# Optimization experiments

Measured on AMD Instinct MI355X. Metric: run time of the kernel, lower is better.

Reference implementation:

```python
import jax, jax.numpy as jnp
import numpy as np

N, T, E, H, V = 32768, 20, 50, 50, 200
PAD = 0

def setup_inputs() -> dict:
    key = jax.random.key(0)
    ks = jax.random.split(key, 11)
    s = 1.0 / np.sqrt(H)  # torch LSTM init scale
    return {
        "char_indices": jax.random.randint(ks[0], (N, T), 0, V, dtype=jnp.int32),
        "word_lengths": jax.random.randint(ks[1], (N,), 0, T + 1, dtype=jnp.int32),
        "emb": jax.random.normal(ks[2], (V, E), jnp.float32) * 0.1,
        "W_ih_f": jax.random.normal(ks[3], (4 * H, E), jnp.float32) * s,
        "W_hh_f": jax.random.normal(ks[4], (4 * H, H), jnp.float32) * s,
        "b_ih_f": jax.random.normal(ks[5], (4 * H,), jnp.float32) * s,
        "b_hh_f": jax.random.normal(ks[6], (4 * H,), jnp.float32) * s,
        "W_ih_b": jax.random.normal(ks[7], (4 * H, E), jnp.float32) * s,
        "W_hh_b": jax.random.normal(ks[8], (4 * H, H), jnp.float32) * s,
        "b_ih_b": jax.random.normal(ks[9], (4 * H,), jnp.float32) * s,
        "b_hh_b": jax.random.normal(ks[10], (4 * H,), jnp.float32) * s,
    }

def _run_dir(x, lengths, W_ih, W_hh, b_ih, b_hh, reverse):
    # x: [N,T,E]; returns final hidden state [N,H] at the word's true boundary.
    n = x.shape[0]
    xg = jnp.einsum('nte,ge->ntg', x, W_ih) + b_ih + b_hh  # [N,T,4H]
    def step(carry, t):
        h, c = carry
        g = xg[:, t] + h @ W_hh.T  # [N,4H]
        i, f, gg, o = jnp.split(g, 4, axis=-1)
        c_new = jax.nn.sigmoid(f) * c + jax.nn.sigmoid(i) * jnp.tanh(gg)
        h_new = jax.nn.sigmoid(o) * jnp.tanh(c_new)
        valid = (t < lengths)[:, None]  # only update inside the word
        return (jnp.where(valid, h_new, h), jnp.where(valid, c_new, c)), None
    ts = jnp.arange(T - 1, -1, -1) if reverse else jnp.arange(T)
    z = jnp.zeros((n, W_hh.shape[1]), x.dtype)
    (h, _), _ = jax.lax.scan(step, (z, z), ts)
    return h

def reference(char_indices, word_lengths, emb, W_ih_f, W_hh_f, b_ih_f, b_hh_f,
              W_ih_b, W_hh_b, b_ih_b, b_hh_b):
    emb = emb.at[PAD].set(0.0)  # padding_idx row is zero
    x = emb[char_indices]  # [N,T,E]
    h_f = _run_dir(x, word_lengths, W_ih_f, W_hh_f, b_ih_f, b_hh_f, reverse=False)
    h_b = _run_dir(x, word_lengths, W_ih_b, W_hh_b, b_ih_b, b_hh_b, reverse=True)
    return jnp.concatenate([h_f, h_b], axis=-1)  # [N, 2H]
```

## Files before the change

### kernel.cpp

```cpp
#include <hip/hip_runtime.h>


#define TT    20
#define HH    50
#define VV    200
#define TILES 13
#define GSTR  212
#define GSH   (VV * GSTR)
#define WSH   (TILES * 16 * 64)
#define NW    32768
#define NB_G  332
#define NB_W  104
#define NB_H  128
#define NBLK  4096

#define N2LOG2E (-1.4426950408889634f)
#define P2LOG2E 2.8853900817779268f

typedef __attribute__((ext_vector_type(8))) short bf16x8;
typedef __attribute__((ext_vector_type(4))) short s16x4;
typedef __attribute__((ext_vector_type(4))) float f32x4;

__device__ __forceinline__ float frcp(float x) { return __builtin_amdgcn_rcpf(x); }
#if __has_builtin(__builtin_amdgcn_exp2f)
__device__ __forceinline__ float fexp2(float x) { return __builtin_amdgcn_exp2f(x); }
#else
__device__ __forceinline__ float fexp2(float x) { return exp2f(x); }
#endif

__device__ __forceinline__ short f2bf(float x) {
    unsigned b = __builtin_bit_cast(unsigned, x);
    unsigned r = (b + 0x7FFFu + ((b >> 16) & 1u)) >> 16;
    return (short)r;
}
__device__ __forceinline__ float bf2f(short s) {
    return __builtin_bit_cast(float, ((unsigned)(unsigned short)s) << 16);
}

__global__ void k_prep(const float* __restrict__ emb,
                       const float* __restrict__ Wih_f, const float* __restrict__ bih_f,
                       const float* __restrict__ bhh_f,
                       const float* __restrict__ Wih_b, const float* __restrict__ bih_b,
                       const float* __restrict__ bhh_b,
                       const float* __restrict__ Whh_f, const float* __restrict__ Whh_b,
                       const int* __restrict__ lens,
                       short* __restrict__ Gimg, short* __restrict__ Wimg,
                       int* __restrict__ cnt) {
    int blk = blockIdx.x;
    int tid = threadIdx.x;
    if (blk < NB_G) {
        int idx = blk * 256 + tid;
        if (idx >= 2 * GSH) return;
        int d = idx / GSH;
        int rem = idx % GSH;
        int v = rem / GSTR;
        int u = (rem % GSTR) >> 2;
        int g = idx & 3;
        if (u >= HH) { Gimg[idx] = 0; return; }
        int r = g * HH + u;
        const float* Wih = d ? Wih_b : Wih_f;
        const float* bih = d ? bih_b : bih_f;
        const float* bhh = d ? bhh_b : bhh_f;
        float s = bih[r] + bhh[r];
        if (v != 0) {
            #pragma unroll 10
            for (int e = 0; e < HH; ++e) s = fmaf(emb[v * HH + e], Wih[r * HH + e], s);
        }
        float sc = (g == 2) ? P2LOG2E : N2LOG2E;
        Gimg[idx] = f2bf(s * sc);
    } else if (blk < NB_G + NB_W) {
        int idx = (blk - NB_G) * 256 + tid;
        if (idx >= 2 * WSH) return;
        int d = idx / WSH;
        int e = idx % WSH;
        int t = e >> 10, m = (e >> 6) & 15, k = e & 63;
        int u = 4 * t + (m >> 2), g = m & 3;
        const float* Whh = d ? Whh_b : Whh_f;
        float sc = (g == 2) ? P2LOG2E : N2LOG2E;
        float val = (k < HH && u < HH) ? Whh[(g * HH + u) * HH + k] * sc : 0.0f;
        int ksw = (k & 7) | (((k >> 3) ^ (m & 7)) << 3);
        Wimg[d * WSH + (e & ~63) + ksw] = f2bf(val);
    } else {
        int hb = blk - NB_G - NB_W;
        __shared__ int hcnt[21];
        if (tid < 21) hcnt[tid] = 0;
        __syncthreads();
        atomicAdd(&hcnt[lens[hb * 256 + tid]], 1);
        __syncthreads();
        if (tid < 21) cnt[hb * 21 + tid] = hcnt[tid];
    }
}

__global__ void k_scat(const int* __restrict__ lens, const int* __restrict__ cnt,
                       int* __restrict__ perm) {
    __shared__ int lcnt[NB_H * 21];
    __shared__ int part[8][21];
    __shared__ int tot[21];
    __shared__ int cur[21];
    int b = blockIdx.x, t = threadIdx.x;
    for (int i = t; i < NB_H * 21; i += 256) lcnt[i] = cnt[i];
    __syncthreads();
    if (t < 168) {
        int L = t % 21, c = t / 21;
        int s = 0;
        for (int bb = c * 16; bb < c * 16 + 16; ++bb) s += lcnt[bb * 21 + L];
        part[c][L] = s;
    }
    __syncthreads();
    if (t < 21) {
        int a = 0;
        #pragma unroll
        for (int c = 0; c < 8; ++c) a += part[c][t];
        tot[t] = a;
    }
    __syncthreads();
    if (t < 21) {
        int a = 0;
        for (int L2 = 20; L2 > t; --L2) a += tot[L2];
        for (int bb = 0; bb < b; ++bb) a += lcnt[bb * 21 + t];
        cur[t] = a;
    }
    __syncthreads();
    int i = b * 256 + t;
    int pos = atomicAdd(&cur[lens[i]], 1);
    perm[pos] = i;
}

__launch_bounds__(512, 6)
__global__ void k_lstm(const int* __restrict__ chars, const int* __restrict__ lens,
                       const int* __restrict__ perm,
                       const short* __restrict__ Gimg, const short* __restrict__ Wimg,
                       float* __restrict__ out) {
    __shared__ __align__(16) short hs[2][1024];
    __shared__ unsigned char cs[16 * TT];

    int gb   = blockIdx.x;
    int d    = gb & 1;
    int grp  = gb >> 1;
    int tid  = threadIdx.x;
    int lane = tid & 63;
    int wv   = __builtin_amdgcn_readfirstlane(tid >> 6);
    int quad = lane >> 4;
    int n    = lane & 15;
    int x7   = n & 7;
    int slotbase = grp * 16;

    {
        int4 z = {0, 0, 0, 0};
        int4* hz = (int4*)&hs[0][0];
        if (tid < 256) hz[tid] = z;
    }
    for (int i = tid; i < 16 * TT; i += 512) {
        int w = perm[slotbase + i / TT];
        cs[i] = (unsigned char)chars[w * TT + i % TT];
    }

    int word = perm[slotbase + n];
    int L = lens[word];
    int mL = L;
    #pragma unroll
    for (int off = 8; off; off >>= 1) {
        int t2 = __shfl_xor(mL, off);
        mL = mL > t2 ? mL : t2;
    }
    mL = __builtin_amdgcn_readfirstlane(mL);

    int pa0 = quad ^ x7;
    int pa1 = (quad + 4) ^ x7;

    int tA = wv, tB = wv + 8;
    int nt = (wv < 5) ? 2 : 1;
    int uA = 4 * tA + quad;
    int uB = 4 * tB + quad;
    int hidxA = n * 64 + (((uA >> 3) ^ x7) << 3) + (uA & 7);
    int hidxB = n * 64 + (((uB >> 3) ^ x7) << 3) + (uB & 7);

    const short* Wd = Wimg + d * WSH;
    bf16x8 A0a = *(const bf16x8*)(Wd + (tA * 16 + n) * 64 + pa0 * 8);
    bf16x8 A1a = *(const bf16x8*)(Wd + (tA * 16 + n) * 64 + pa1 * 8);
    bf16x8 A0b, A1b;
    if (nt == 2) {
        A0b = *(const bf16x8*)(Wd + (tB * 16 + n) * 64 + pa0 * 8);
        A1b = *(const bf16x8*)(Wd + (tB * 16 + n) * 64 + pa1 * 8);
    }

    const short* Gg = Gimg + d * GSH;
    const unsigned char* cw = cs + n * TT;

    float cstA = 0.0f, hfA = 0.0f, cstB = 0.0f, hfB = 0.0f;

    __syncthreads();

    int vcur = cw[(d && L > 0) ? (L - 1) : 0];
    int cur = 0;

    #pragma unroll 1
    for (int s = 0; s < mL; ++s) {
        bool valid = s < L;

        const short* gvp = Gg + vcur * GSTR + quad * 4;
        s16x4 gvA = *(const s16x4*)(gvp + tA * 16);
        s16x4 gvB;
        if (nt == 2) gvB = *(const s16x4*)(gvp + tB * 16);

        const short* hb = hs[cur];
        bf16x8 B0 = *(const bf16x8*)(hb + n * 64 + pa0 * 8);
        bf16x8 B1 = *(const bf16x8*)(hb + n * 64 + pa1 * 8);

        int sn = s + 1;
        int pn = (sn < L) ? (d ? (L - 1 - sn) : sn) : 0;
        vcur = cw[pn];

        f32x4 aA;
        aA[0] = bf2f(gvA[0]); aA[1] = bf2f(gvA[1]);
        aA[2] = bf2f(gvA[2]); aA[3] = bf2f(gvA[3]);
        aA = __builtin_amdgcn_mfma_f32_16x16x32_bf16(A0a, B0, aA, 0, 0, 0);
        aA = __builtin_amdgcn_mfma_f32_16x16x32_bf16(A1a, B1, aA, 0, 0, 0);
        f32x4 aB;
        if (nt == 2) {
            aB[0] = bf2f(gvB[0]); aB[1] = bf2f(gvB[1]);
            aB[2] = bf2f(gvB[2]); aB[3] = bf2f(gvB[3]);
            aB = __builtin_amdgcn_mfma_f32_16x16x32_bf16(A0b, B0, aB, 0, 0, 0);
            aB = __builtin_amdgcn_mfma_f32_16x16x32_bf16(A1b, B1, aB, 0, 0, 0);
        }

        {
            float ig = frcp(1.0f + fexp2(aA[0]));
            float fg = frcp(1.0f + fexp2(aA[1]));
            float tg = 1.0f - 2.0f * frcp(1.0f + fexp2(aA[2]));
            float og = frcp(1.0f + fexp2(aA[3]));
            float cn = fg * cstA + ig * tg;
            float hn = og * (1.0f - 2.0f * frcp(1.0f + fexp2(cn * P2LOG2E)));
            bool upd = valid && (uA < HH);
            cstA = upd ? cn : cstA;
            hfA  = upd ? hn : hfA;
        }
        if (nt == 2) {
            float ig = frcp(1.0f + fexp2(aB[0]));
            float fg = frcp(1.0f + fexp2(aB[1]));
            float tg = 1.0f - 2.0f * frcp(1.0f + fexp2(aB[2]));
            float og = frcp(1.0f + fexp2(aB[3]));
            float cn = fg * cstB + ig * tg;
            float hn = og * (1.0f - 2.0f * frcp(1.0f + fexp2(cn * P2LOG2E)));
            bool upd = valid && (uB < HH);
            cstB = upd ? cn : cstB;
            hfB  = upd ? hn : hfB;
        }

        short* hnb = hs[cur ^ 1];
        if (uA < HH) hnb[hidxA] = f2bf(hfA);
        if (nt == 2 && uB < HH) hnb[hidxB] = f2bf(hfB);
        __syncthreads();
        cur ^= 1;
    }

    float* orow = out + (size_t)word * (2 * HH) + d * HH;
    if (uA < HH) orow[uA] = hfA;
    if (nt == 2 && uB < HH) orow[uB] = hfB;
}

extern "C" void kernel_launch(void* const* d_in, const int* in_sizes, int n_in,
                              void* d_out, int out_size, void* d_ws, size_t ws_size,
                              hipStream_t stream) {
    const int*   chars = (const int*)d_in[0];
    const int*   lens  = (const int*)d_in[1];
    const float* emb   = (const float*)d_in[2];
    const float* Wih_f = (const float*)d_in[3];
    const float* Whh_f = (const float*)d_in[4];
    const float* bih_f = (const float*)d_in[5];
    const float* bhh_f = (const float*)d_in[6];
    const float* Wih_b = (const float*)d_in[7];
    const float* Whh_b = (const float*)d_in[8];
    const float* bih_b = (const float*)d_in[9];
    const float* bhh_b = (const float*)d_in[10];
    float* out = (float*)d_out;

    short* Gimg = (short*)d_ws;
    short* Wimg = Gimg + 2 * GSH;
    int*   cnt  = (int*)(Wimg + 2 * WSH);
    int*   perm = cnt + NB_H * 21;

    k_prep<<<NB_G + NB_W + NB_H, 256, 0, stream>>>(emb, Wih_f, bih_f, bhh_f,
                                                   Wih_b, bih_b, bhh_b,
                                                   Whh_f, Whh_b, lens,
                                                   Gimg, Wimg, cnt);
    k_scat<<<NB_H, 256, 0, stream>>>(lens, cnt, perm);
    k_lstm<<<NBLK, 512, 0, stream>>>(chars, lens, perm, Gimg, Wimg, out);
}
```

Measured before the change: 146.3 us.

## Merge prep and scatter kernels via cooperative grid sync; resize LSTM blocks to 7 waves

The prep and scatter kernels become a single cooperative kernel that uses a grid-wide sync between histogram building and the permutation scatter, removing one launch. The LSTM kernel now runs 7 waves per block instead of 8, with the 13 hidden-unit tiles redistributed (tB = wv+7, six waves take two tiles) and launch bounds of 448 threads, 7 blocks. This aims to cut launch gaps and improve occupancy or balance, but the grid sync costs something and the cooperative launch needs all 564 blocks resident at once.

```diff
diff --git a/kernel.cpp b/kernel.cpp
--- a/kernel.cpp
+++ b/kernel.cpp
@@ -1,4 +1,5 @@
 #include <hip/hip_runtime.h>
+#include <hip/hip_cooperative_groups.h>
 
 
 #define TT    20
@@ -37,96 +38,103 @@
     return __builtin_bit_cast(float, ((unsigned)(unsigned short)s) << 16);
 }
 
-__global__ void k_prep(const float* __restrict__ emb,
-                       const float* __restrict__ Wih_f, const float* __restrict__ bih_f,
-                       const float* __restrict__ bhh_f,
-                       const float* __restrict__ Wih_b, const float* __restrict__ bih_b,
-                       const float* __restrict__ bhh_b,
-                       const float* __restrict__ Whh_f, const float* __restrict__ Whh_b,
-                       const int* __restrict__ lens,
-                       short* __restrict__ Gimg, short* __restrict__ Wimg,
-                       int* __restrict__ cnt) {
+__global__ void k_pre(const float* __restrict__ emb,
+                      const float* __restrict__ Wih_f, const float* __restrict__ bih_f,
+                      const float* __restrict__ bhh_f,
+                      const float* __restrict__ Wih_b, const float* __restrict__ bih_b,
+                      const float* __restrict__ bhh_b,
+                      const float* __restrict__ Whh_f, const float* __restrict__ Whh_b,
+                      const int* __restrict__ lens,
+                      short* __restrict__ Gimg, short* __restrict__ Wimg,
+                      int* __restrict__ cnt, int* __restrict__ perm) {
     int blk = blockIdx.x;
     int tid = threadIdx.x;
-    if (blk < NB_G) {
-        int idx = blk * 256 + tid;
-        if (idx >= 2 * GSH) return;
-        int d = idx / GSH;
-        int rem = idx % GSH;
-        int v = rem / GSTR;
-        int u = (rem % GSTR) >> 2;
-        int g = idx & 3;
-        if (u >= HH) { Gimg[idx] = 0; return; }
-        int r = g * HH + u;
-        const float* Wih = d ? Wih_b : Wih_f;
-        const float* bih = d ? bih_b : bih_f;
-        const float* bhh = d ? bhh_b : bhh_f;
-        float s = bih[r] + bhh[r];
-        if (v != 0) {
-            #pragma unroll 10
-            for (int e = 0; e < HH; ++e) s = fmaf(emb[v * HH + e], Wih[r * HH + e], s);
-        }
-        float sc = (g == 2) ? P2LOG2E : N2LOG2E;
-        Gimg[idx] = f2bf(s * sc);
-    } else if (blk < NB_G + NB_W) {
-        int idx = (blk - NB_G) * 256 + tid;
-        if (idx >= 2 * WSH) return;
-        int d = idx / WSH;
-        int e = idx % WSH;
-        int t = e >> 10, m = (e >> 6) & 15, k = e & 63;
-        int u = 4 * t + (m >> 2), g = m & 3;
-        const float* Whh = d ? Whh_b : Whh_f;
-        float sc = (g == 2) ? P2LOG2E : N2LOG2E;
-        float val = (k < HH && u < HH) ? Whh[(g * HH + u) * HH + k] * sc : 0.0f;
-        int ksw = (k & 7) | (((k >> 3) ^ (m & 7)) << 3);
-        Wimg[d * WSH + (e & ~63) + ksw] = f2bf(val);
-    } else {
-        int hb = blk - NB_G - NB_W;
-        __shared__ int hcnt[21];
-        if (tid < 21) hcnt[tid] = 0;
-        __syncthreads();
-        atomicAdd(&hcnt[lens[hb * 256 + tid]], 1);
-        __syncthreads();
-        if (tid < 21) cnt[hb * 21 + tid] = hcnt[tid];
-    }
-}
-
-__global__ void k_scat(const int* __restrict__ lens, const int* __restrict__ cnt,
-                       int* __restrict__ perm) {
     __shared__ int lcnt[NB_H * 21];
     __shared__ int part[8][21];
     __shared__ int tot[21];
     __shared__ int cur[21];
-    int b = blockIdx.x, t = threadIdx.x;
-    for (int i = t; i < NB_H * 21; i += 256) lcnt[i] = cnt[i];
-    __syncthreads();
-    if (t < 168) {
-        int L = t % 21, c = t / 21;
-        int s = 0;
-        for (int bb = c * 16; bb < c * 16 + 16; ++bb) s += lcnt[bb * 21 + L];
-        part[c][L] = s;
-    }
-    __syncthreads();
-    if (t < 21) {
-        int a = 0;
-        #pragma unroll
-        for (int c = 0; c < 8; ++c) a += part[c][t];
-        tot[t] = a;
-    }
-    __syncthreads();
-    if (t < 21) {
-        int a = 0;
-        for (int L2 = 20; L2 > t; --L2) a += tot[L2];
-        for (int bb = 0; bb < b; ++bb) a += lcnt[bb * 21 + t];
-        cur[t] = a;
-    }
-    __syncthreads();
-    int i = b * 256 + t;
-    int pos = atomicAdd(&cur[lens[i]], 1);
-    perm[pos] = i;
-}
-
-__launch_bounds__(512, 6)
+
+    if (blk < NB_G) {
+        int idx = blk * 256 + tid;
+        if (idx < 2 * GSH) {
+            int d = idx / GSH;
+            int rem = idx % GSH;
+            int v = rem / GSTR;
+            int u = (rem % GSTR) >> 2;
+            int g = idx & 3;
+            if (u >= HH) {
+                Gimg[idx] = 0;
+            } else {
+                int r = g * HH + u;
+                const float* Wih = d ? Wih_b : Wih_f;
+                const float* bih = d ? bih_b : bih_f;
+                const float* bhh = d ? bhh_b : bhh_f;
+                float s = bih[r] + bhh[r];
+                if (v != 0) {
+                    #pragma unroll 10
+                    for (int e = 0; e < HH; ++e)
+                        s = fmaf(emb[v * HH + e], Wih[r * HH + e], s);
+                }
+                float sc = (g == 2) ? P2LOG2E : N2LOG2E;
+                Gimg[idx] = f2bf(s * sc);
+            }
+        }
+    } else if (blk < NB_G + NB_W) {
+        int idx = (blk - NB_G) * 256 + tid;
+        if (idx < 2 * WSH) {
+            int d = idx / WSH;
+            int e = idx % WSH;
+            int t = e >> 10, m = (e >> 6) & 15, k = e & 63;
+            int u = 4 * t + (m >> 2), g = m & 3;
+            const float* Whh = d ? Whh_b : Whh_f;
+            float sc = (g == 2) ? P2LOG2E : N2LOG2E;
+            float val = (k < HH && u < HH) ? Whh[(g * HH + u) * HH + k] * sc : 0.0f;
+            int ksw = (k & 7) | (((k >> 3) ^ (m & 7)) << 3);
+            Wimg[d * WSH + (e & ~63) + ksw] = f2bf(val);
+        }
+    } else {
+        int hb = blk - NB_G - NB_W;
+        if (tid < 21) lcnt[tid] = 0;
+        __syncthreads();
+        atomicAdd(&lcnt[lens[hb * 256 + tid]], 1);
+        __syncthreads();
+        if (tid < 21) cnt[hb * 21 + tid] = lcnt[tid];
+    }
+
+    cooperative_groups::this_grid().sync();
+
+    if (blk < NB_H) {
+        int b = blk, t = tid;
+        for (int i = t; i < NB_H * 21; i += 256) lcnt[i] = cnt[i];
+        __syncthreads();
+        if (t < 168) {
+            int L = t % 21, c = t / 21;
+            int s = 0;
+            for (int bb = c * 16; bb < c * 16 + 16; ++bb) s += lcnt[bb * 21 + L];
+            part[c][L] = s;
+        }
+        __syncthreads();
+        if (t < 21) {
+            int a = 0;
+            #pragma unroll
+            for (int c2 = 0; c2 < 8; ++c2) a += part[c2][t];
+            tot[t] = a;
+        }
+        __syncthreads();
+        if (t < 21) {
+            int a = 0;
+            for (int L2 = 20; L2 > t; --L2) a += tot[L2];
+            for (int bb = 0; bb < b; ++bb) a += lcnt[bb * 21 + t];
+            cur[t] = a;
+        }
+        __syncthreads();
+        int i = b * 256 + t;
+        int pos = atomicAdd(&cur[lens[i]], 1);
+        perm[pos] = i;
+    }
+}
+
+__launch_bounds__(448, 7)
 __global__ void k_lstm(const int* __restrict__ chars, const int* __restrict__ lens,
                        const int* __restrict__ perm,
                        const short* __restrict__ Gimg, const short* __restrict__ Wimg,
@@ -147,10 +155,9 @@
 
     {
         int4 z = {0, 0, 0, 0};
-        int4* hz = (int4*)&hs[0][0];
-        if (tid < 256) hz[tid] = z;
-    }
-    for (int i = tid; i < 16 * TT; i += 512) {
+        if (tid < 256) ((int4*)&hs[0][0])[tid] = z;
+    }
+    for (int i = tid; i < 16 * TT; i += 448) {
         int w = perm[slotbase + i / TT];
         cs[i] = (unsigned char)chars[w * TT + i % TT];
     }
@@ -168,8 +175,8 @@
     int pa0 = quad ^ x7;
     int pa1 = (quad + 4) ^ x7;
 
-    int tA = wv, tB = wv + 8;
-    int nt = (wv < 5) ? 2 : 1;
+    int tA = wv, tB = wv + 7;
+    int nt = (wv < 6) ? 2 : 1;
     int uA = 4 * tA + quad;
     int uB = 4 * tB + quad;
     int hidxA = n * 64 + (((uA >> 3) ^ x7) << 3) + (uA & 7);
@@ -280,10 +287,15 @@
     int*   cnt  = (int*)(Wimg + 2 * WSH);
     int*   perm = cnt + NB_H * 21;
 
-    k_prep<<<NB_G + NB_W + NB_H, 256, 0, stream>>>(emb, Wih_f, bih_f, bhh_f,
-                                                   Wih_b, bih_b, bhh_b,
-                                                   Whh_f, Whh_b, lens,
-                                                   Gimg, Wimg, cnt);
-    k_scat<<<NB_H, 256, 0, stream>>>(lens, cnt, perm);
-    k_lstm<<<NBLK, 512, 0, stream>>>(chars, lens, perm, Gimg, Wimg, out);
-}
+    void* args[14] = {
+        (void*)&emb,
+        (void*)&Wih_f, (void*)&bih_f, (void*)&bhh_f,
+        (void*)&Wih_b, (void*)&bih_b, (void*)&bhh_b,
+        (void*)&Whh_f, (void*)&Whh_b,
+        (void*)&lens,
+        (void*)&Gimg, (void*)&Wimg, (void*)&cnt, (void*)&perm
+    };
+    hipLaunchCooperativeKernel((void*)k_pre, dim3(NB_G + NB_W + NB_H), dim3(256),
+                               args, 0, stream);
+    k_lstm<<<NBLK, 448, 0, stream>>>(chars, lens, perm, Gimg, Wimg, out);
+}
```

New measurement: 249.3 us. 1.7x slower.

## Store gate table in fp32, prefetch next step's gates, stage Wih in LDS

Applied to the files above, without the earlier changes.

The precomputed input-gate table becomes fp32 instead of bf16, which drops the per-step bf16-to-float conversion. The next timestep's gate vector is now loaded before the activation math so its latency overlaps with compute. Character offsets are pre-multiplied by the row stride and stored as 16-bit values in shared memory. The prep kernel is reorganised so each block stages W_ih in LDS and computes 8 vocab rows per thread, cutting its block count. In exchange the gate table doubles in size and register pressure rises from holding the prefetched gates.

```diff
diff --git a/kernel.cpp b/kernel.cpp
--- a/kernel.cpp
+++ b/kernel.cpp
@@ -5,11 +5,11 @@
 #define HH    50
 #define VV    200
 #define TILES 13
-#define GSTR  212
-#define GSH   (VV * GSTR)
+#define GSTRF 212
+#define GS32  (VV * GSTRF)
 #define WSH   (TILES * 16 * 64)
 #define NW    32768
-#define NB_G  332
+#define NB_G  50
 #define NB_W  104
 #define NB_H  128
 #define NBLK  4096
@@ -18,7 +18,6 @@
 #define P2LOG2E 2.8853900817779268f
 
 typedef __attribute__((ext_vector_type(8))) short bf16x8;
-typedef __attribute__((ext_vector_type(4))) short s16x4;
 typedef __attribute__((ext_vector_type(4))) float f32x4;
 
 __device__ __forceinline__ float frcp(float x) { return __builtin_amdgcn_rcpf(x); }
@@ -32,9 +31,6 @@
     unsigned b = __builtin_bit_cast(unsigned, x);
     unsigned r = (b + 0x7FFFu + ((b >> 16) & 1u)) >> 16;
     return (short)r;
-}
-__device__ __forceinline__ float bf2f(short s) {
-    return __builtin_bit_cast(float, ((unsigned)(unsigned short)s) << 16);
 }
 
 __global__ void k_prep(const float* __restrict__ emb,
@@ -44,30 +40,50 @@
                        const float* __restrict__ bhh_b,
                        const float* __restrict__ Whh_f, const float* __restrict__ Whh_b,
                        const int* __restrict__ lens,
-                       short* __restrict__ Gimg, short* __restrict__ Wimg,
+                       float* __restrict__ G32, short* __restrict__ Wimg,
                        int* __restrict__ cnt) {
     int blk = blockIdx.x;
     int tid = threadIdx.x;
+    __shared__ float Wl[4 * HH * HH];
+    __shared__ float bs[4 * HH];
+
     if (blk < NB_G) {
-        int idx = blk * 256 + tid;
-        if (idx >= 2 * GSH) return;
-        int d = idx / GSH;
-        int rem = idx % GSH;
-        int v = rem / GSTR;
-        int u = (rem % GSTR) >> 2;
-        int g = idx & 3;
-        if (u >= HH) { Gimg[idx] = 0; return; }
-        int r = g * HH + u;
+        int d = blk / 25;
+        int vbase = (blk % 25) * 8;
         const float* Wih = d ? Wih_b : Wih_f;
         const float* bih = d ? bih_b : bih_f;
         const float* bhh = d ? bhh_b : bhh_f;
-        float s = bih[r] + bhh[r];
-        if (v != 0) {
-            #pragma unroll 10
-            for (int e = 0; e < HH; ++e) s = fmaf(emb[v * HH + e], Wih[r * HH + e], s);
-        }
-        float sc = (g == 2) ? P2LOG2E : N2LOG2E;
-        Gimg[idx] = f2bf(s * sc);
+        for (int i = tid; i < 4 * HH * HH; i += 256) Wl[i] = Wih[i];
+        if (tid < 4 * HH) {
+            int g = tid / HH;
+            float sc = (g == 2) ? P2LOG2E : N2LOG2E;
+            bs[tid] = (bih[tid] + bhh[tid]) * sc;
+        }
+        __syncthreads();
+        int r = tid;
+        if (r < 4 * HH) {
+            int g = r / HH, u = r % HH;
+            float sc = (g == 2) ? P2LOG2E : N2LOG2E;
+            #pragma unroll
+            for (int vv = 0; vv < 8; ++vv) {
+                int v = vbase + vv;
+                float s = bs[r];
+                if (v != 0) {
+                    #pragma unroll 10
+                    for (int e = 0; e < HH; ++e)
+                        s = fmaf(emb[v * HH + e] * sc, Wl[r * HH + e], s);
+                }
+                G32[d * GS32 + v * GSTRF + u * 4 + g] = s;
+            }
+        } else {
+            int idx = r - 4 * HH;
+            for (int k = idx; k < 8 * 12; k += 56) {
+                int v = vbase + k / 12;
+                int rem = k % 12;
+                int u = HH + rem / 4, g = rem & 3;
+                G32[d * GS32 + v * GSTRF + u * 4 + g] = 0.0f;
+            }
+        }
     } else if (blk < NB_G + NB_W) {
         int idx = (blk - NB_G) * 256 + tid;
         if (idx >= 2 * WSH) return;
@@ -129,10 +145,10 @@
 __launch_bounds__(512, 6)
 __global__ void k_lstm(const int* __restrict__ chars, const int* __restrict__ lens,
                        const int* __restrict__ perm,
-                       const short* __restrict__ Gimg, const short* __restrict__ Wimg,
+                       const float* __restrict__ G32, const short* __restrict__ Wimg,
                        float* __restrict__ out) {
     __shared__ __align__(16) short hs[2][1024];
-    __shared__ unsigned char cs[16 * TT];
+    __shared__ unsigned short cs[16 * TT];
 
     int gb   = blockIdx.x;
     int d    = gb & 1;
@@ -147,12 +163,11 @@
 
     {
         int4 z = {0, 0, 0, 0};
-        int4* hz = (int4*)&hs[0][0];
-        if (tid < 256) hz[tid] = z;
+        if (tid < 256) ((int4*)&hs[0][0])[tid] = z;
     }
     for (int i = tid; i < 16 * TT; i += 512) {
         int w = perm[slotbase + i / TT];
-        cs[i] = (unsigned char)chars[w * TT + i % TT];
+        cs[i] = (unsigned short)(chars[w * TT + i % TT] * GSTRF);
     }
 
     int word = perm[slotbase + n];
@@ -184,45 +199,43 @@
         A1b = *(const bf16x8*)(Wd + (tB * 16 + n) * 64 + pa1 * 8);
     }
 
-    const short* Gg = Gimg + d * GSH;
-    const unsigned char* cw = cs + n * TT;
+    const float* Gd = G32 + d * GS32 + quad * 4;
+    const unsigned short* cw = cs + n * TT;
 
     float cstA = 0.0f, hfA = 0.0f, cstB = 0.0f, hfB = 0.0f;
 
     __syncthreads();
 
-    int vcur = cw[(d && L > 0) ? (L - 1) : 0];
+    int off0 = cw[(d && L > 0) ? (L - 1) : 0];
+    f32x4 gA = *(const f32x4*)(Gd + off0 + tA * 16);
+    f32x4 gB;
+    if (nt == 2) gB = *(const f32x4*)(Gd + off0 + tB * 16);
     int cur = 0;
 
     #pragma unroll 1
     for (int s = 0; s < mL; ++s) {
         bool valid = s < L;
 
-        const short* gvp = Gg + vcur * GSTR + quad * 4;
-        s16x4 gvA = *(const s16x4*)(gvp + tA * 16);
-        s16x4 gvB;
-        if (nt == 2) gvB = *(const s16x4*)(gvp + tB * 16);
-
         const short* hb = hs[cur];
         bf16x8 B0 = *(const bf16x8*)(hb + n * 64 + pa0 * 8);
         bf16x8 B1 = *(const bf16x8*)(hb + n * 64 + pa1 * 8);
 
         int sn = s + 1;
         int pn = (sn < L) ? (d ? (L - 1 - sn) : sn) : 0;
-        vcur = cw[pn];
-
-        f32x4 aA;
-        aA[0] = bf2f(gvA[0]); aA[1] = bf2f(gvA[1]);
-        aA[2] = bf2f(gvA[2]); aA[3] = bf2f(gvA[3]);
+        int offn = cw[pn];
+
+        f32x4 aA = gA;
         aA = __builtin_amdgcn_mfma_f32_16x16x32_bf16(A0a, B0, aA, 0, 0, 0);
         aA = __builtin_amdgcn_mfma_f32_16x16x32_bf16(A1a, B1, aA, 0, 0, 0);
         f32x4 aB;
         if (nt == 2) {
-            aB[0] = bf2f(gvB[0]); aB[1] = bf2f(gvB[1]);
-            aB[2] = bf2f(gvB[2]); aB[3] = bf2f(gvB[3]);
+            aB = gB;
             aB = __builtin_amdgcn_mfma_f32_16x16x32_bf16(A0b, B0, aB, 0, 0, 0);
             aB = __builtin_amdgcn_mfma_f32_16x16x32_bf16(A1b, B1, aB, 0, 0, 0);
         }
+
+        gA = *(const f32x4*)(Gd + offn + tA * 16);
+        if (nt == 2) gB = *(const f32x4*)(Gd + offn + tB * 16);
 
         {
             float ig = frcp(1.0f + fexp2(aA[0]));
@@ -275,15 +288,15 @@
     const float* bhh_b = (const float*)d_in[10];
     float* out = (float*)d_out;
 
-    short* Gimg = (short*)d_ws;
-    short* Wimg = Gimg + 2 * GSH;
+    float* G32 = (float*)d_ws;
+    short* Wimg = (short*)(G32 + 2 * GS32);
     int*   cnt  = (int*)(Wimg + 2 * WSH);
     int*   perm = cnt + NB_H * 21;
 
     k_prep<<<NB_G + NB_W + NB_H, 256, 0, stream>>>(emb, Wih_f, bih_f, bhh_f,
                                                    Wih_b, bih_b, bhh_b,
                                                    Whh_f, Whh_b, lens,
-                                                   Gimg, Wimg, cnt);
+                                                   G32, Wimg, cnt);
     k_scat<<<NB_H, 256, 0, stream>>>(lens, cnt, perm);
-    k_lstm<<<NBLK, 512, 0, stream>>>(chars, lens, perm, Gimg, Wimg, out);
-}
+    k_lstm<<<NBLK, 512, 0, stream>>>(chars, lens, perm, G32, Wimg, out);
+}
```

Result: slower. 156.4 us (+6.9%).
